# Kernel optimization log

Hardware: AMD Instinct MI355X
Metric: run time of the kernel (lower is better)

Reference implementation:

```python
import jax, jax.numpy as jnp
import numpy as np

B, T, P, C, H = 2, 2048, 2048, 1024, 16  # batch, new tokens, cached tokens, n_embd, n_head
HD = C // H  # head_dim = 64


def setup_inputs() -> dict:
    key = jax.random.key(0)
    ks = jax.random.split(key, 5)
    return {
        "x": jax.random.normal(ks[0], (B, T, C), dtype=jnp.float32),
        "k_cache": jax.random.normal(ks[1], (B, P, C), dtype=jnp.float32),
        "v_cache": jax.random.normal(ks[2], (B, P, C), dtype=jnp.float32),
        "W_attn": jax.random.normal(ks[3], (C, 3 * C), dtype=jnp.float32) * 0.02,
        "W_proj": jax.random.normal(ks[4], (C, C), dtype=jnp.float32) * 0.02,
    }


def reference(x, k_cache, v_cache, W_attn, W_proj):
    # c_attn (no bias): qkv projection, then split into q, k_rem, v_rem
    qkv = x @ W_attn                      # [B, T, 3C]
    q, k_rem, v_rem = jnp.split(qkv, 3, axis=2)
    # KV-cache concat along time
    k_full = jnp.concatenate([k_cache, k_rem], axis=1)  # [B, S, C], S = P + T
    v_full = jnp.concatenate([v_cache, v_rem], axis=1)
    S = P + T
    # reshape to heads
    qh = q.reshape(B, T, H, HD).transpose(0, 2, 1, 3)       # [B, H, T, HD]
    kh = k_full.reshape(B, S, H, HD).transpose(0, 2, 1, 3)  # [B, H, S, HD]
    vh = v_full.reshape(B, S, H, HD).transpose(0, 2, 1, 3)  # [B, H, S, HD]
    # full attention matrix (module explicitly disables flash)
    att = jnp.einsum("bhqd,bhkd->bhqk", qh, kh) * (1.0 / np.sqrt(HD))  # [B,H,T,S]
    # cache-offset causal mask: query global position = P + i attends to key j <= P + i
    mask = jnp.arange(S)[None, :] <= (P + jnp.arange(T))[:, None]  # [T, S]
    att = jnp.where(mask[None, None], att, -jnp.inf)
    att = jax.nn.softmax(att, axis=-1)
    # dropout p=0.0 (inference) -> no-op
    y = jnp.einsum("bhqk,bhkd->bhqd", att, vh)  # [B, H, T, HD]
    y = y.transpose(0, 2, 1, 3).reshape(B, T, C)
    y = y @ W_proj  # c_proj, no bias; resid dropout p=0 -> no-op
    return (y, k_full, v_full)
```

## Files before the change

kernel.cpp:

```cpp
#include <hip/hip_runtime.h>

#define BB 2
#define TT 2048
#define PP 2048
#define CC 1024
#define HH 16
#define SS 4096

typedef unsigned short u16;
typedef unsigned int u32;
typedef __attribute__((ext_vector_type(8))) short s16x8;
typedef __attribute__((ext_vector_type(4))) float f32x4;
typedef __attribute__((ext_vector_type(4))) unsigned short u16x4;

#define GLOAD16(g, l)                                                                   \
  __builtin_amdgcn_global_load_lds((const __attribute__((address_space(1))) u32*)(g),   \
                                   (__attribute__((address_space(3))) u32*)(l), 16, 0, 0)

#define QSCALE 0.18033688011112042f

__device__ __forceinline__ u16 f2bf(float f) {
  unsigned u = __float_as_uint(f);
  u += 0x7fff + ((u >> 16) & 1);
  return (u16)(u >> 16);
}

__device__ __forceinline__ u16 p2bf(float f) {
  return (u16)((__float_as_uint(f) + 0x8000u) >> 16);
}

__global__ __launch_bounds__(256) void cvt_f32_bf16(const float* __restrict__ src,
                                                    u16* __restrict__ dst) {
  size_t i = ((size_t)blockIdx.x * 256 + threadIdx.x) * 4;
  f32x4 v = *(const f32x4*)(src + i);
  u16x4 o = { f2bf(v[0]), f2bf(v[1]), f2bf(v[2]), f2bf(v[3]) };
  *(u16x4*)(dst + i) = o;
}

__global__ __launch_bounds__(256) void transpose_w_bf16(const float* __restrict__ src,
                                                        u16* __restrict__ dst,
                                                        int rows, int cols) {
  __shared__ float tile[64][65];
  int r0 = blockIdx.y * 64, c0 = blockIdx.x * 64;
  int tx = threadIdx.x & 63, ty = threadIdx.x >> 6;
#pragma unroll
  for (int i = 0; i < 16; i++) {
    int r = ty + i * 4;
    tile[r][tx] = src[(size_t)(r0 + r) * cols + c0 + tx];
  }
  __syncthreads();
#pragma unroll
  for (int i = 0; i < 16; i++) {
    int cc = ty + i * 4;
    dst[(size_t)(c0 + cc) * rows + r0 + tx] = f2bf(tile[tx][cc]);
  }
}

__global__ __launch_bounds__(256) void cache_copy(const float* __restrict__ kc,
                                                  const float* __restrict__ vc,
                                                  float* __restrict__ kf,
                                                  float* __restrict__ vf,
                                                  u16* __restrict__ kb) {
  size_t flat = ((size_t)blockIdx.x * 256 + threadIdx.x) * 4;
  int b = (int)(flat >> 21);
  size_t dsto = flat + (size_t)b * (TT * CC);
  f32x4 kv = *(const f32x4*)(kc + flat);
  f32x4 vv = *(const f32x4*)(vc + flat);
  *(f32x4*)(kf + dsto) = kv;
  *(f32x4*)(vf + dsto) = vv;
  u16x4 k4 = { f2bf(kv[0]), f2bf(kv[1]), f2bf(kv[2]), f2bf(kv[3]) };
  *(u16x4*)(kb + dsto) = k4;
}

__global__ __launch_bounds__(256) void vT_cache_kernel(const float* __restrict__ vc,
                                                       u16* __restrict__ vTb) {
  __shared__ float tile[64][65];
  int bh = blockIdx.y, b = bh >> 4, h = bh & 15;
  int p0 = blockIdx.x * 64;
  int tx = threadIdx.x & 63, ty = threadIdx.x >> 6;
#pragma unroll
  for (int i = 0; i < 16; i++) {
    int p = ty + i * 4;
    tile[p][tx] = vc[(size_t)(b * PP + p0 + p) * CC + h * 64 + tx];
  }
  __syncthreads();
#pragma unroll
  for (int i = 0; i < 16; i++) {
    int d = ty + i * 4;
    vTb[(size_t)((b * HH + h) * 64 + d) * SS + p0 + tx] = f2bf(tile[tx][d]);
  }
}

__global__ __launch_bounds__(256) void vT_rem_kernel(const float* __restrict__ vf,
                                                     u16* __restrict__ vTb) {
  __shared__ float tile[64][65];
  int bh = blockIdx.y, b = bh >> 4, h = bh & 15;
  int p0 = blockIdx.x * 64;
  int tx = threadIdx.x & 63, ty = threadIdx.x >> 6;
#pragma unroll
  for (int i = 0; i < 16; i++) {
    int p = ty + i * 4;
    tile[p][tx] = vf[(size_t)(b * SS + PP + p0 + p) * CC + h * 64 + tx];
  }
  __syncthreads();
#pragma unroll
  for (int i = 0; i < 16; i++) {
    int d = ty + i * 4;
    vTb[(size_t)((b * HH + h) * 64 + d) * SS + PP + p0 + tx] = f2bf(tile[tx][d]);
  }
}

__global__ __launch_bounds__(256) void gemm_bt(const u16* __restrict__ A,
                                               const u16* __restrict__ BT,
                                               int N, int mode,
                                               float* __restrict__ out0,
                                               u16* __restrict__ qb,
                                               float* __restrict__ kf,
                                               u16* __restrict__ kb,
                                               float* __restrict__ vf) {
  __shared__ u16 As[128 * 64];
  __shared__ u16 Bs[128 * 64];
  const int m0 = blockIdx.y * 128, n0 = blockIdx.x * 128;
  const int tid = threadIdx.x, lane = tid & 63, wave = tid >> 6;
  const int wm = wave & 1, wn = wave >> 1;
  const int c = lane & 15, quad = lane >> 4;
  const int srow = lane >> 3;
  const int scol = (lane & 7) ^ (srow & 7);
  const int rkey = (c & 7) << 3;

  f32x4 acc[4][4] = {};

  for (int k0 = 0; k0 < 1024; k0 += 64) {
    __syncthreads();
#pragma unroll
    for (int it = 0; it < 4; it++) {
      int chunk = it * 4 + wave;
      int row = chunk * 8 + srow;
      GLOAD16(A + (size_t)(m0 + row) * 1024 + k0 + scol * 8, &As[chunk * 512]);
      GLOAD16(BT + (size_t)(n0 + row) * 1024 + k0 + scol * 8, &Bs[chunk * 512]);
    }
    __syncthreads();
#pragma unroll
    for (int kc = 0; kc < 64; kc += 32) {
      s16x8 af[4], bf[4];
#pragma unroll
      for (int i = 0; i < 4; i++) {
        af[i] = *(const s16x8*)&As[(((wm * 64 + i * 16 + c) << 6) + kc + quad * 8) ^ rkey];
        bf[i] = *(const s16x8*)&Bs[(((wn * 64 + i * 16 + c) << 6) + kc + quad * 8) ^ rkey];
      }
#pragma unroll
      for (int mi = 0; mi < 4; mi++)
#pragma unroll
        for (int ni = 0; ni < 4; ni++)
          acc[mi][ni] = __builtin_amdgcn_mfma_f32_16x16x32_bf16(af[mi], bf[ni], acc[mi][ni], 0, 0, 0);
    }
  }

#pragma unroll
  for (int mi = 0; mi < 4; mi++) {
#pragma unroll
    for (int ni = 0; ni < 4; ni++) {
      f32x4 v = acc[mi][ni];
      int gmb = m0 + wm * 64 + mi * 16 + quad * 4;
      int gn = n0 + wn * 64 + ni * 16 + c;
      if (mode == 0) {
#pragma unroll
        for (int r = 0; r < 4; r++)
          out0[(size_t)(gmb + r) * N + gn] = v[r];
      } else {
        int region = n0 >> 10;
        if (region == 0) {
#pragma unroll
          for (int r = 0; r < 4; r++)
            qb[(size_t)(gmb + r) * 1024 + gn] = f2bf(v[r] * QSCALE);
        } else if (region == 1) {
          int ccol = gn - 1024;
#pragma unroll
          for (int r = 0; r < 4; r++) {
            int gm = gmb + r, b = gm >> 11, t = gm & 2047;
            size_t off = (size_t)b * (SS * CC) + (size_t)(PP + t) * CC + ccol;
            kf[off] = v[r];
            kb[off] = f2bf(v[r]);
          }
        } else {
          int ccol = gn - 2048;
#pragma unroll
          for (int r = 0; r < 4; r++) {
            int gm = gmb + r, b = gm >> 11, t = gm & 2047;
            vf[(size_t)b * (SS * CC) + (size_t)(PP + t) * CC + ccol] = v[r];
          }
        }
      }
    }
  }
}

__global__ __launch_bounds__(512, 4) void attn_kernel(const u16* __restrict__ qb,
                                                      const u16* __restrict__ kb,
                                                      const u16* __restrict__ vT,
                                                      u16* __restrict__ yb) {
  __shared__ u16 Ks[2][64 * 64];
  __shared__ u16 Vs[2][64 * 64];
  __shared__ u16 Ps[8][16 * 64];
  const int L = blockIdx.x;
  const int xcd = L & 7, rest = L >> 3;
  const int qt = 15 - (rest >> 2);
  const int bh = (xcd << 2) | (rest & 3);
  const int b = bh >> 4, h = bh & 15;
  const int q0 = qt * 128;
  const int tid = threadIdx.x, lane = tid & 63, wave = tid >> 6;
  const int c = lane & 15, quad = lane >> 4;
  const int srow = lane >> 3;
  const int scol = (lane & 7) ^ (srow & 7);
  const int rkey = (c & 7) << 3;

  const int s_end = PP + q0 + 128;

  const u16* kg = kb + (size_t)(b * SS + wave * 8 + srow) * 1024 + h * 64 + scol * 8;
  const u16* vg = vT + ((size_t)bh * 64 + wave * 8 + srow) * SS + scol * 8;

  GLOAD16(kg, &Ks[0][wave * 512]);
  GLOAD16(vg, &Vs[0][wave * 512]);

  const short ov = (c == 0) ? (short)0x3F80 : (short)0;
  const s16x8 ones = { ov, ov, ov, ov, ov, ov, ov, ov };

  s16x8 qf[2];
  {
    int qr = q0 + wave * 16 + c;
    qf[0] = *(const s16x8*)(qb + (size_t)(b * TT + qr) * 1024 + h * 64 + quad * 8);
    qf[1] = *(const s16x8*)(qb + (size_t)(b * TT + qr) * 1024 + h * 64 + 32 + quad * 8);
  }

  f32x4 o[5] = {};
  float m = -1e30f;
  u16* Pw = Ps[wave];

  int cur = 0;
  for (int s0 = 0; s0 < s_end; s0 += 64, cur ^= 1) {
    __syncthreads();

    if (s0 + 64 < s_end) {
      GLOAD16(kg + (size_t)(s0 + 64) * 1024, &Ks[cur ^ 1][wave * 512]);
      GLOAD16(vg + (s0 + 64), &Vs[cur ^ 1][wave * 512]);
    }

    const u16* Kc = Ks[cur];
    const u16* Vc = Vs[cur];

    f32x4 sc[4];
    __builtin_amdgcn_s_setprio(1);
#pragma unroll
    for (int nt = 0; nt < 4; nt++) {
      s16x8 kf0 = *(const s16x8*)&Kc[(((nt * 16 + c) << 6) + quad * 8) ^ rkey];
      s16x8 kf1 = *(const s16x8*)&Kc[(((nt * 16 + c) << 6) + 32 + quad * 8) ^ rkey];
      f32x4 z = { 0.f, 0.f, 0.f, 0.f };
      z = __builtin_amdgcn_mfma_f32_16x16x32_bf16(qf[0], kf0, z, 0, 0, 0);
      z = __builtin_amdgcn_mfma_f32_16x16x32_bf16(qf[1], kf1, z, 0, 0, 0);
      sc[nt] = z;
    }
    __builtin_amdgcn_s_setprio(0);

    s16x8 vf0[4], vf1[4];
#pragma unroll
    for (int dt = 0; dt < 4; dt++) {
      vf0[dt] = *(const s16x8*)&Vc[(((dt * 16 + c) << 6) + quad * 8) ^ rkey];
      vf1[dt] = *(const s16x8*)&Vc[(((dt * 16 + c) << 6) + 32 + quad * 8) ^ rkey];
    }

    const int diag = s0 - (PP + q0);
    if (diag >= 0) {
#pragma unroll
      for (int nt = 0; nt < 4; nt++) {
        int col = nt * 16 + c + diag;
#pragma unroll
        for (int r = 0; r < 4; r++) {
          int rq = wave * 16 + quad * 4 + r;
          if (col > rq) sc[nt][r] = -1e30f;
        }
      }
    }

    float lm = -1e30f;
#pragma unroll
    for (int nt = 0; nt < 4; nt++)
      lm = fmaxf(lm, fmaxf(fmaxf(sc[nt][0], sc[nt][1]),
                           fmaxf(sc[nt][2], sc[nt][3])));
    if (__any(lm > m + 8.0f)) {
#pragma unroll
      for (int off = 1; off < 64; off <<= 1)
        lm = fmaxf(lm, __shfl_xor(lm, off, 64));
      float alpha = __builtin_amdgcn_exp2f(m - lm);
      m = lm;
#pragma unroll
      for (int dt = 0; dt < 5; dt++)
#pragma unroll
        for (int r = 0; r < 4; r++) o[dt][r] *= alpha;
    }

#pragma unroll
    for (int nt = 0; nt < 4; nt++)
#pragma unroll
      for (int r = 0; r < 4; r++)
        Pw[(((quad * 4 + r) << 6) + nt * 16 + c) ^ (quad << 4)] =
            p2bf(__builtin_amdgcn_exp2f(sc[nt][r] - m));
    const int pkey = (c >> 2) << 4;
    s16x8 pa0 = *(const s16x8*)&Pw[((c << 6) + quad * 8) ^ pkey];
    s16x8 pa1 = *(const s16x8*)&Pw[((c << 6) + 32 + quad * 8) ^ pkey];

    __builtin_amdgcn_s_setprio(1);
#pragma unroll
    for (int dt = 0; dt < 4; dt++) {
      o[dt] = __builtin_amdgcn_mfma_f32_16x16x32_bf16(pa0, vf0[dt], o[dt], 0, 0, 0);
      o[dt] = __builtin_amdgcn_mfma_f32_16x16x32_bf16(pa1, vf1[dt], o[dt], 0, 0, 0);
    }
    o[4] = __builtin_amdgcn_mfma_f32_16x16x32_bf16(pa0, ones, o[4], 0, 0, 0);
    o[4] = __builtin_amdgcn_mfma_f32_16x16x32_bf16(pa1, ones, o[4], 0, 0, 0);
    __builtin_amdgcn_s_setprio(0);
  }

#pragma unroll
  for (int r = 0; r < 4; r++) {
    float l = __shfl(o[4][r], (lane & 48), 64);
    float inv = 1.0f / l;
    int qr = q0 + wave * 16 + quad * 4 + r;
#pragma unroll
    for (int dt = 0; dt < 4; dt++)
      yb[(size_t)(b * TT + qr) * 1024 + h * 64 + dt * 16 + c] = f2bf(o[dt][r] * inv);
  }
}

extern "C" void kernel_launch(void* const* d_in, const int* in_sizes, int n_in,
                              void* d_out, int out_size, void* d_ws, size_t ws_size,
                              hipStream_t stream) {
  const float* x       = (const float*)d_in[0];
  const float* k_cache = (const float*)d_in[1];
  const float* v_cache = (const float*)d_in[2];
  const float* W_attn  = (const float*)d_in[3];
  const float* W_proj  = (const float*)d_in[4];

  float* out_y = (float*)d_out;
  float* out_k = out_y + (size_t)BB * TT * CC;
  float* out_v = out_k + (size_t)BB * SS * CC;

  u16* xb  = (u16*)d_ws;
  u16* WaT = xb  + 4194304;
  u16* WpT = WaT + 3145728;
  u16* qb  = WpT + 1048576;
  u16* kb  = qb  + 4194304;
  u16* vT  = kb  + 8388608;
  u16* yb  = vT  + 8388608;

  cvt_f32_bf16<<<dim3(4096), dim3(256), 0, stream>>>(x, xb);
  transpose_w_bf16<<<dim3(48, 16), dim3(256), 0, stream>>>(W_attn, WaT, 1024, 3072);
  transpose_w_bf16<<<dim3(16, 16), dim3(256), 0, stream>>>(W_proj, WpT, 1024, 1024);
  cache_copy<<<dim3(4096), dim3(256), 0, stream>>>(k_cache, v_cache, out_k, out_v, kb);
  vT_cache_kernel<<<dim3(32, 32), dim3(256), 0, stream>>>(v_cache, vT);
  gemm_bt<<<dim3(24, 32), dim3(256), 0, stream>>>(xb, WaT, 3072, 1, nullptr, qb, out_k, kb, out_v);
  vT_rem_kernel<<<dim3(32, 32), dim3(256), 0, stream>>>(out_v, vT);
  attn_kernel<<<dim3(512), dim3(512), 0, stream>>>(qb, kb, vT, yb);
  gemm_bt<<<dim3(8, 32), dim3(256), 0, stream>>>(yb, WpT, 1024, 0, out_y, nullptr, nullptr, nullptr, nullptr);
}
```

Measured before the change: 316.7 us.

## Fuse cache copy with V transpose, use 64-row proj GEMM, rebalance attention order

Merges the KV-cache copy and bf16 conversion kernel with the V-cache transpose kernel, so v_cache is read once and one launch is saved. The output projection moves to a new 64x128-tile GEMM kernel, doubling the block count to fill more compute units. The attention tile ordering now interleaves heavy and light causal query tiles for better load balance. The fused kernel writes k and v with scalar 4-byte stores instead of 16-byte vector stores, which may lower write efficiency.

```diff
diff --git a/kernel.cpp b/kernel.cpp
--- a/kernel.cpp
+++ b/kernel.cpp
@@ -56,24 +56,12 @@
   }
 }
 
-__global__ __launch_bounds__(256) void cache_copy(const float* __restrict__ kc,
+__global__ __launch_bounds__(256) void cache_prep(const float* __restrict__ kc,
                                                   const float* __restrict__ vc,
                                                   float* __restrict__ kf,
                                                   float* __restrict__ vf,
-                                                  u16* __restrict__ kb) {
-  size_t flat = ((size_t)blockIdx.x * 256 + threadIdx.x) * 4;
-  int b = (int)(flat >> 21);
-  size_t dsto = flat + (size_t)b * (TT * CC);
-  f32x4 kv = *(const f32x4*)(kc + flat);
-  f32x4 vv = *(const f32x4*)(vc + flat);
-  *(f32x4*)(kf + dsto) = kv;
-  *(f32x4*)(vf + dsto) = vv;
-  u16x4 k4 = { f2bf(kv[0]), f2bf(kv[1]), f2bf(kv[2]), f2bf(kv[3]) };
-  *(u16x4*)(kb + dsto) = k4;
-}
-
-__global__ __launch_bounds__(256) void vT_cache_kernel(const float* __restrict__ vc,
-                                                       u16* __restrict__ vTb) {
+                                                  u16* __restrict__ kb,
+                                                  u16* __restrict__ vTb) {
   __shared__ float tile[64][65];
   int bh = blockIdx.y, b = bh >> 4, h = bh & 15;
   int p0 = blockIdx.x * 64;
@@ -81,7 +69,14 @@
 #pragma unroll
   for (int i = 0; i < 16; i++) {
     int p = ty + i * 4;
-    tile[p][tx] = vc[(size_t)(b * PP + p0 + p) * CC + h * 64 + tx];
+    size_t src = (size_t)(b * PP + p0 + p) * CC + h * 64 + tx;
+    size_t dst = (size_t)(b * SS + p0 + p) * CC + h * 64 + tx;
+    float kv = kc[src];
+    float vv = vc[src];
+    kf[dst] = kv;
+    vf[dst] = vv;
+    kb[dst] = f2bf(kv);
+    tile[p][tx] = vv;
   }
   __syncthreads();
 #pragma unroll
@@ -195,6 +190,64 @@
   }
 }
 
+__global__ __launch_bounds__(256) void gemm_bt64(const u16* __restrict__ A,
+                                                 const u16* __restrict__ BT,
+                                                 float* __restrict__ out0) {
+  __shared__ u16 As[64 * 64];
+  __shared__ u16 Bs[128 * 64];
+  const int m0 = blockIdx.y * 64, n0 = blockIdx.x * 128;
+  const int tid = threadIdx.x, lane = tid & 63, wave = tid >> 6;
+  const int wm = wave & 1, wn = wave >> 1;
+  const int c = lane & 15, quad = lane >> 4;
+  const int srow = lane >> 3;
+  const int scol = (lane & 7) ^ (srow & 7);
+  const int rkey = (c & 7) << 3;
+
+  f32x4 acc[2][4] = {};
+
+  for (int k0 = 0; k0 < 1024; k0 += 64) {
+    __syncthreads();
+#pragma unroll
+    for (int it = 0; it < 6; it++) {
+      int idx = it * 4 + wave;
+      if (idx < 8)
+        GLOAD16(A + (size_t)(m0 + idx * 8 + srow) * 1024 + k0 + scol * 8, &As[idx * 512]);
+      else
+        GLOAD16(BT + (size_t)(n0 + (idx - 8) * 8 + srow) * 1024 + k0 + scol * 8,
+                &Bs[(idx - 8) * 512]);
+    }
+    __syncthreads();
+#pragma unroll
+    for (int kc = 0; kc < 64; kc += 32) {
+      s16x8 af[2], bf[4];
+#pragma unroll
+      for (int i = 0; i < 2; i++)
+        af[i] = *(const s16x8*)&As[(((wm * 32 + i * 16 + c) << 6) + kc + quad * 8) ^ rkey];
+#pragma unroll
+      for (int i = 0; i < 4; i++)
+        bf[i] = *(const s16x8*)&Bs[(((wn * 64 + i * 16 + c) << 6) + kc + quad * 8) ^ rkey];
+#pragma unroll
+      for (int mi = 0; mi < 2; mi++)
+#pragma unroll
+        for (int ni = 0; ni < 4; ni++)
+          acc[mi][ni] = __builtin_amdgcn_mfma_f32_16x16x32_bf16(af[mi], bf[ni], acc[mi][ni], 0, 0, 0);
+    }
+  }
+
+#pragma unroll
+  for (int mi = 0; mi < 2; mi++) {
+#pragma unroll
+    for (int ni = 0; ni < 4; ni++) {
+      f32x4 v = acc[mi][ni];
+      int gmb = m0 + wm * 32 + mi * 16 + quad * 4;
+      int gn = n0 + wn * 64 + ni * 16 + c;
+#pragma unroll
+      for (int r = 0; r < 4; r++)
+        out0[(size_t)(gmb + r) * 1024 + gn] = v[r];
+    }
+  }
+}
+
 __global__ __launch_bounds__(512, 4) void attn_kernel(const u16* __restrict__ qb,
                                                       const u16* __restrict__ kb,
                                                       const u16* __restrict__ vT,
@@ -204,7 +257,8 @@
   __shared__ u16 Ps[8][16 * 64];
   const int L = blockIdx.x;
   const int xcd = L & 7, rest = L >> 3;
-  const int qt = 15 - (rest >> 2);
+  const int h16 = rest >> 2;
+  const int qt = (h16 < 8) ? (15 - h16) : (h16 - 8);
   const int bh = (xcd << 2) | (rest & 3);
   const int b = bh >> 4, h = bh & 15;
   const int q0 = qt * 128;
@@ -354,10 +408,9 @@
   cvt_f32_bf16<<<dim3(4096), dim3(256), 0, stream>>>(x, xb);
   transpose_w_bf16<<<dim3(48, 16), dim3(256), 0, stream>>>(W_attn, WaT, 1024, 3072);
   transpose_w_bf16<<<dim3(16, 16), dim3(256), 0, stream>>>(W_proj, WpT, 1024, 1024);
-  cache_copy<<<dim3(4096), dim3(256), 0, stream>>>(k_cache, v_cache, out_k, out_v, kb);
-  vT_cache_kernel<<<dim3(32, 32), dim3(256), 0, stream>>>(v_cache, vT);
+  cache_prep<<<dim3(32, 32), dim3(256), 0, stream>>>(k_cache, v_cache, out_k, out_v, kb, vT);
   gemm_bt<<<dim3(24, 32), dim3(256), 0, stream>>>(xb, WaT, 3072, 1, nullptr, qb, out_k, kb, out_v);
   vT_rem_kernel<<<dim3(32, 32), dim3(256), 0, stream>>>(out_v, vT);
   attn_kernel<<<dim3(512), dim3(512), 0, stream>>>(qb, kb, vT, yb);
-  gemm_bt<<<dim3(8, 32), dim3(256), 0, stream>>>(yb, WpT, 1024, 0, out_y, nullptr, nullptr, nullptr, nullptr);
-}
+  gemm_bt64<<<dim3(8, 64), dim3(256), 0, stream>>>(yb, WpT, out_y);
+}
```

Measured after the change: 305.9 us. 1.04x faster.
